# Kernel tuning notes

Measured on AMD Instinct MI355X. Metric: run time of the kernel, lower is better.

## Reference

```python
import jax, jax.numpy as jnp
import numpy as np

N = 50000      # nodes
R = 3          # relation types
E = 200000     # edges per relation
DIN, DHID, DOUT = 128, 128, 64


def _hetero_graphconv(x, src, dst, W, b):
    """Sum over relations of dgl GraphConv(norm='both') applied per relation.
    x:[N,d_in], src/dst:[R,E], W:[R,d_in,d_out], b:[R,d_out] -> [N,d_out]"""
    Rr, Ee = src.shape
    n = x.shape[0]
    off = (jnp.arange(Rr) * n)[:, None]            # per-relation segment offset
    src_f = (src + off).reshape(-1)                # [R*E]
    dst_f = (dst + off).reshape(-1)
    ones = jnp.ones((Rr * Ee,), x.dtype)
    out_deg = jax.ops.segment_sum(ones, src_f, num_segments=Rr * n).reshape(Rr, n)
    in_deg = jax.ops.segment_sum(ones, dst_f, num_segments=Rr * n).reshape(Rr, n)
    out_norm = jnp.maximum(out_deg, 1.0) ** -0.5   # dgl clamps deg to min 1
    in_norm = jnp.maximum(in_deg, 1.0) ** -0.5
    # gather src features, scaled by per-relation out-degree norm: [R,E,d_in]
    msgs = x[src] * jnp.take_along_axis(out_norm, src, axis=1)[..., None]
    agg = jax.ops.segment_sum(msgs.reshape(Rr * Ee, -1), dst_f,
                              num_segments=Rr * n).reshape(Rr, n, -1)
    agg = agg * in_norm[..., None]                 # [R,N,d_in]
    # per-relation linear then sum over relations (HeteroGraphConv 'sum')
    return jnp.einsum('rnd,rdo->no', agg, W) + b.sum(axis=0)


def setup_inputs() -> dict:
    key = jax.random.key(0)
    ks = jax.random.split(key, 7)
    x = jax.random.normal(ks[0], (N, DIN), jnp.float32)
    src = jax.random.randint(ks[1], (R, E), 0, N)
    dst = jax.random.randint(ks[2], (R, E), 0, N)
    W1 = jax.random.normal(ks[3], (R, DIN, DHID), jnp.float32) / np.sqrt(DIN).astype(np.float32)
    b1 = jax.random.normal(ks[4], (R, DHID), jnp.float32) * 0.01
    W2 = jax.random.normal(ks[5], (R, DHID, DOUT), jnp.float32) / np.sqrt(DHID).astype(np.float32)
    b2 = jax.random.normal(ks[6], (R, DOUT), jnp.float32) * 0.01
    return {"x": x, "W1": W1, "b1": b1, "W2": W2, "b2": b2, "src": src, "dst": dst}


def reference(x, W1, b1, W2, b2, src, dst):
    h = jax.nn.relu(_hetero_graphconv(x, src, dst, W1, b1))
    return _hetero_graphconv(h, src, dst, W2, b2)
```

## Files before the change

### kernel.cpp

```cpp
#include <hip/hip_runtime.h>

#define N_NODES 50000
#define N_REL   3
#define N_EDGE  200000
#define RN      (N_REL * N_NODES)
#define RE      (N_REL * N_EDGE)
#define GEMM1_BLKS 782
#define DEG_BLKS   2344
#define SCAN_BLOCKS 49
#define FUSE_CHUNKS 98

typedef short bf16x8 __attribute__((ext_vector_type(8)));
typedef float f32x4  __attribute__((ext_vector_type(4)));

__device__ __forceinline__ unsigned short f2bf(float f) {
    unsigned u = __float_as_uint(f);
    u = (u + 0x7fffu + ((u >> 16) & 1u)) >> 16;
    return (unsigned short)u;
}
__device__ __forceinline__ unsigned pack_bf2(float lo, float hi) {
    return (unsigned)f2bf(lo) | ((unsigned)f2bf(hi) << 16);
}

__device__ __forceinline__ void wtrans_one(
    const float* __restrict__ W, unsigned short* __restrict__ Wtf, int ncols, int i)
{
    int rel = i / (128 * ncols);
    int rem = i - rel * 128 * ncols;
    int k   = rem / ncols;
    int n   = rem - k * ncols;
    int f   = (rel * (ncols / 16) + (n >> 4)) * 4 + (k >> 5);
    int idx = f * 512 + ((k & 31) >> 3) * 128 + (n & 15) * 8 + (k & 7);
    Wtf[idx] = f2bf(W[i]);
}

__global__ __launch_bounds__(256) void wtrans2_kernel(
    const float* __restrict__ W1, unsigned short* __restrict__ Wt1,
    const float* __restrict__ W2, unsigned short* __restrict__ Wt2)
{
    int i = blockIdx.x * 256 + threadIdx.x;
    if (i < 3 * 128 * 128) {
        wtrans_one(W1, Wt1, 128, i);
    } else {
        int j = i - 3 * 128 * 128;
        if (j < 3 * 128 * 64) wtrans_one(W2, Wt2, 64, j);
    }
}

template <bool ABF16, int NCOLS>
__device__ __forceinline__ void gemm_body(
    const void* __restrict__ Av, const unsigned short* __restrict__ Wtf,
    unsigned short* __restrict__ Y, int nrows, int mt,
    unsigned* As, unsigned* Ws0, unsigned* Ws1)
{
    const int tid = threadIdx.x;
    const uint4* Wt4 = (const uint4*)Wtf;

    if constexpr (ABF16) {
        const uint4* Ab = (const uint4*)Av;
        #pragma unroll
        for (int p = 0; p < 4; ++p) {
            int q   = p * 256 + tid;
            int row = q >> 4, w4 = q & 15;
            int gr  = mt + row;
            uint4 v = make_uint4(0u, 0u, 0u, 0u);
            if (gr < nrows) v = Ab[(size_t)gr * 16 + w4];
            As[row * 68 + w4 * 4 + 0] = v.x;
            As[row * 68 + w4 * 4 + 1] = v.y;
            As[row * 68 + w4 * 4 + 2] = v.z;
            As[row * 68 + w4 * 4 + 3] = v.w;
        }
    } else {
        const float* A = (const float*)Av;
        #pragma unroll
        for (int p = 0; p < 16; ++p) {
            int q   = tid + p * 256;
            int row = q >> 6, wc = q & 63;
            int gr  = mt + row;
            float2 v = make_float2(0.f, 0.f);
            if (gr < nrows) v = *reinterpret_cast<const float2*>(&A[(size_t)gr * 128 + wc * 2]);
            As[row * 68 + wc] = pack_bf2(v.x, v.y);
        }
    }

    #pragma unroll
    for (int p = 0; p < 4; ++p) {
        uint4 v = Wt4[tid + p * 256];
        *reinterpret_cast<uint4*>(&Ws0[(tid + p * 256) * 4]) = v;
    }
    __syncthreads();

    const int w  = tid >> 6;
    const int l  = tid & 63;
    const int g  = l >> 4;
    const int lr = l & 15;
    const int ar = w * 16 + lr;

    bf16x8 a[4];
    #pragma unroll
    for (int kb = 0; kb < 4; ++kb)
        a[kb] = *reinterpret_cast<const bf16x8*>(&As[ar * 68 + kb * 16 + g * 4]);

    constexpr int TPR  = NCOLS / 16;
    constexpr int NGRP = 3 * NCOLS / 64;
    const int boff = (g * 16 + lr) * 4;

    unsigned* wc_buf = Ws0;
    unsigned* wn_buf = Ws1;
    #pragma unroll 1
    for (int grp = 0; grp < NGRP; ++grp) {
        uint4 st[4];
        if (grp + 1 < NGRP) {
            #pragma unroll
            for (int p = 0; p < 4; ++p)
                st[p] = Wt4[(grp + 1) * 1024 + tid + p * 256];
        }

        f32x4 acc[4];
        #pragma unroll
        for (int ct4 = 0; ct4 < 4; ++ct4) {
            acc[ct4] = (f32x4){0.f, 0.f, 0.f, 0.f};
            #pragma unroll
            for (int kb = 0; kb < 4; ++kb) {
                bf16x8 b = *reinterpret_cast<const bf16x8*>(
                    &wc_buf[(ct4 * 4 + kb) * 256 + boff]);
                acc[ct4] = __builtin_amdgcn_mfma_f32_16x16x32_bf16(a[kb], b, acc[ct4], 0, 0, 0);
            }
        }

        int gct0 = grp * 4;
        int rel  = gct0 / TPR;
        int cb   = (gct0 % TPR) * 16;
        #pragma unroll
        for (int i = 0; i < 4; ++i) {
            int grow = mt + w * 16 + g * 4 + i;
            if (grow < nrows) {
                size_t rowbase = ((size_t)rel * N_NODES + grow) * NCOLS + cb;
                #pragma unroll
                for (int ct4 = 0; ct4 < 4; ++ct4)
                    Y[rowbase + ct4 * 16 + lr] = f2bf(acc[ct4][i]);
            }
        }

        if (grp + 1 < NGRP) {
            #pragma unroll
            for (int p = 0; p < 4; ++p)
                *reinterpret_cast<uint4*>(&wn_buf[(tid + p * 256) * 4]) = st[p];
        }
        __syncthreads();
        unsigned* t = wc_buf; wc_buf = wn_buf; wn_buf = t;
    }
}

template <bool ABF16, int NCOLS>
__global__ __launch_bounds__(256) void gemm_mfma(
    const void* __restrict__ Av, const unsigned short* __restrict__ Wtf,
    unsigned short* __restrict__ Y, int nrows)
{
    __shared__ unsigned As[64 * 68];
    __shared__ unsigned Ws[2][4096];
    gemm_body<ABF16, NCOLS>(Av, Wtf, Y, nrows, blockIdx.x * 64, As, Ws[0], Ws[1]);
}

__device__ __forceinline__ void gemm1_body_light(
    const float* __restrict__ A, const unsigned short* __restrict__ Wtf,
    unsigned short* __restrict__ Y, int mt, unsigned* Ws)
{
    const int tid = threadIdx.x;
    const uint4* Wt4 = (const uint4*)Wtf;
    const int w  = tid >> 6;
    const int l  = tid & 63;
    const int g  = l >> 4;
    const int lr = l & 15;
    const int arow = mt + w * 16 + lr;
    const bool rowok = arow < N_NODES;

    bf16x8 a[4];
    #pragma unroll
    for (int kb = 0; kb < 4; ++kb) {
        float4 v0 = make_float4(0.f, 0.f, 0.f, 0.f);
        float4 v1 = make_float4(0.f, 0.f, 0.f, 0.f);
        if (rowok) {
            const float* ap = &A[(size_t)arow * 128 + kb * 32 + g * 8];
            v0 = *reinterpret_cast<const float4*>(ap);
            v1 = *reinterpret_cast<const float4*>(ap + 4);
        }
        union { unsigned u[4]; bf16x8 v; } cv;
        cv.u[0] = pack_bf2(v0.x, v0.y);
        cv.u[1] = pack_bf2(v0.z, v0.w);
        cv.u[2] = pack_bf2(v1.x, v1.y);
        cv.u[3] = pack_bf2(v1.z, v1.w);
        a[kb] = cv.v;
    }

    const int boff = (g * 16 + lr) * 4;

    #pragma unroll 1
    for (int grp = 0; grp < 6; ++grp) {
        __syncthreads();
        #pragma unroll
        for (int p = 0; p < 4; ++p) {
            uint4 v = Wt4[grp * 1024 + tid + p * 256];
            *reinterpret_cast<uint4*>(&Ws[(tid + p * 256) * 4]) = v;
        }
        __syncthreads();

        f32x4 acc[4];
        #pragma unroll
        for (int ct4 = 0; ct4 < 4; ++ct4) {
            acc[ct4] = (f32x4){0.f, 0.f, 0.f, 0.f};
            #pragma unroll
            for (int kb = 0; kb < 4; ++kb) {
                bf16x8 b = *reinterpret_cast<const bf16x8*>(
                    &Ws[(ct4 * 4 + kb) * 256 + boff]);
                acc[ct4] = __builtin_amdgcn_mfma_f32_16x16x32_bf16(a[kb], b, acc[ct4], 0, 0, 0);
            }
        }

        int rel = grp >> 1;
        int cb  = (grp & 1) * 64;
        #pragma unroll
        for (int i = 0; i < 4; ++i) {
            int grow = mt + w * 16 + g * 4 + i;
            if (grow < N_NODES) {
                size_t rowbase = ((size_t)rel * N_NODES + grow) * 128 + cb;
                #pragma unroll
                for (int ct4 = 0; ct4 < 4; ++ct4)
                    Y[rowbase + ct4 * 16 + lr] = f2bf(acc[ct4][i]);
            }
        }
    }
}

__global__ __launch_bounds__(256) void fused_gemm1_deg(
    const float* __restrict__ x, const unsigned short* __restrict__ Wt1,
    unsigned short* __restrict__ Y,
    const int* __restrict__ src, const int* __restrict__ dst,
    float* __restrict__ odeg, float* __restrict__ ideg,
    unsigned short* __restrict__ rank)
{
    __shared__ unsigned Ws[4096];

    const int c = blockIdx.x >> 5;
    const int o = blockIdx.x & 31;

    if (o < 8) {
        int gb = c * 8 + o;
        if (gb >= GEMM1_BLKS) return;
        gemm1_body_light(x, Wt1, Y, gb * 64, Ws);
    } else {
        int db = c * 24 + (o - 8);
        int i  = db * 256 + threadIdx.x;
        if (i < RE) {
            int r = i / N_EDGE;
            int s = src[i], t = dst[i];
            unsafeAtomicAdd(&odeg[r * N_NODES + s], 1.0f);
            float old = unsafeAtomicAdd(&ideg[r * N_NODES + t], 1.0f);
            rank[i] = (unsigned short)(int)old;
        }
    }
}

__global__ __launch_bounds__(256) void scan1_kernel(
    const float* __restrict__ ideg, int* __restrict__ off, int* __restrict__ bsums)
{
    __shared__ int tsum[256];
    int tid  = threadIdx.x;
    int base = blockIdx.x * 1024 + tid * 4;
    int c[4], s = 0;
    #pragma unroll
    for (int j = 0; j < 4; ++j) {
        int idx = base + j;
        c[j] = (idx < N_NODES)
             ? (int)(ideg[idx] + ideg[N_NODES + idx] + ideg[2 * N_NODES + idx]) : 0;
        s += c[j];
    }
    tsum[tid] = s;
    __syncthreads();
    #pragma unroll
    for (int d = 1; d < 256; d <<= 1) {
        int v   = tsum[tid];
        int add = (tid >= d) ? tsum[tid - d] : 0;
        __syncthreads();
        tsum[tid] = v + add;
        __syncthreads();
    }
    int run = tsum[tid] - s;
    #pragma unroll
    for (int j = 0; j < 4; ++j) {
        if (base + j < N_NODES) off[base + j] = run;
        run += c[j];
    }
    if (tid == 255) bsums[blockIdx.x] = tsum[255];
}

__global__ __launch_bounds__(256) void scan3_kernel(
    int* __restrict__ off, const int* __restrict__ bsums, int* __restrict__ roff,
    float* __restrict__ odeg, float* __restrict__ ideg)
{
    __shared__ int addsh;
    int tid = threadIdx.x;
    if (tid < 64) {
        int v = (tid < blockIdx.x) ? bsums[tid] : 0;
        #pragma unroll
        for (int d = 32; d > 0; d >>= 1) v += __shfl_down(v, d, 64);
        if (tid == 0) addsh = v;
    }
    __syncthreads();
    int add = addsh;

    int base = blockIdx.x * 1024 + tid * 4;
    #pragma unroll
    for (int j = 0; j < 4; ++j) {
        int t = base + j;
        if (t < N_NODES) {
            int v = off[t] + add;
            off[t] = v;
            float c0 = ideg[t];
            float c1 = ideg[N_NODES + t];
            float c2 = ideg[2 * N_NODES + t];
            roff[t]               = v;
            roff[N_NODES + t]     = v + (int)c0;
            roff[2 * N_NODES + t] = v + (int)(c0 + c1);
            ideg[t]               = rsqrtf(fmaxf(c0, 1.0f));
            ideg[N_NODES + t]     = rsqrtf(fmaxf(c1, 1.0f));
            ideg[2 * N_NODES + t] = rsqrtf(fmaxf(c2, 1.0f));
        }
    }
    if (blockIdx.x == 0 && tid == 0) off[N_NODES] = RE;

    int q0 = blockIdx.x * 256 + tid;
    for (int q = q0; q < RN; q += SCAN_BLOCKS * 256)
        odeg[q] = rsqrtf(fmaxf(odeg[q], 1.0f));
}

__global__ __launch_bounds__(256) void fill_kernel(
    const int* __restrict__ src, const int* __restrict__ dst,
    const float* __restrict__ onorm, const float* __restrict__ inorm,
    const int* __restrict__ roff, const unsigned short* __restrict__ rank,
    int2* __restrict__ csr)
{
    int i = blockIdx.x * 256 + threadIdx.x;
    if (i >= N_EDGE) return;
    int r   = blockIdx.y;
    int idx = r * N_EDGE + i;
    int s = src[idx], t = dst[idx];
    float wv = onorm[r * N_NODES + s] * inorm[r * N_NODES + t];
    int slot = roff[r * N_NODES + t] + (int)rank[idx];
    csr[slot] = make_int2(r * N_NODES + s, __float_as_int(wv));
}

__global__ __launch_bounds__(256) void agg128_kernel(
    const unsigned* __restrict__ Y, const int2* __restrict__ csr,
    const int* __restrict__ off, const float* __restrict__ b, unsigned* __restrict__ hbf)
{
    int wid  = (blockIdx.x * 256 + threadIdx.x) >> 6;
    int lane = threadIdx.x & 63;
    if (wid >= N_NODES) return;

    int e = off[wid], end = off[wid + 1];
    float a0 = 0.f, a1 = 0.f;

    for (; e + 8 <= end; e += 8) {
        int2 p[8]; unsigned y[8];
        #pragma unroll
        for (int j = 0; j < 8; ++j) p[j] = csr[e + j];
        #pragma unroll
        for (int j = 0; j < 8; ++j) y[j] = Y[(size_t)p[j].x * 64 + lane];
        #pragma unroll
        for (int j = 0; j < 8; ++j) {
            float wv = __int_as_float(p[j].y);
            a0 = fmaf(wv, __uint_as_float(y[j] << 16), a0);
            a1 = fmaf(wv, __uint_as_float(y[j] & 0xffff0000u), a1);
        }
    }
    if (e + 4 <= end) {
        int2 p[4]; unsigned y[4];
        #pragma unroll
        for (int j = 0; j < 4; ++j) p[j] = csr[e + j];
        #pragma unroll
        for (int j = 0; j < 4; ++j) y[j] = Y[(size_t)p[j].x * 64 + lane];
        #pragma unroll
        for (int j = 0; j < 4; ++j) {
            float wv = __int_as_float(p[j].y);
            a0 = fmaf(wv, __uint_as_float(y[j] << 16), a0);
            a1 = fmaf(wv, __uint_as_float(y[j] & 0xffff0000u), a1);
        }
        e += 4;
    }
    for (; e < end; ++e) {
        int2 p = csr[e];
        float wv = __int_as_float(p.y);
        unsigned y = Y[(size_t)p.x * 64 + lane];
        a0 = fmaf(wv, __uint_as_float(y << 16), a0);
        a1 = fmaf(wv, __uint_as_float(y & 0xffff0000u), a1);
    }

    int d = lane * 2;
    float o0 = a0 + b[d]     + b[128 + d]     + b[256 + d];
    float o1 = a1 + b[d + 1] + b[128 + d + 1] + b[256 + d + 1];
    hbf[(size_t)wid * 64 + lane] = pack_bf2(fmaxf(o0, 0.f), fmaxf(o1, 0.f));
}

__global__ __launch_bounds__(256) void agg64_kernel(
    const unsigned short* __restrict__ Y, const int2* __restrict__ csr,
    const int* __restrict__ off, const float* __restrict__ b, float* __restrict__ out)
{
    int wid  = (blockIdx.x * 256 + threadIdx.x) >> 6;
    int lane = threadIdx.x & 63;
    if (wid >= N_NODES) return;

    int e = off[wid], end = off[wid + 1];
    float a = 0.f;

    for (; e + 8 <= end; e += 8) {
        int2 p[8]; unsigned short y[8];
        #pragma unroll
        for (int j = 0; j < 8; ++j) p[j] = csr[e + j];
        #pragma unroll
        for (int j = 0; j < 8; ++j) y[j] = Y[(size_t)p[j].x * 64 + lane];
        #pragma unroll
        for (int j = 0; j < 8; ++j)
            a = fmaf(__int_as_float(p[j].y),
                     __uint_as_float(((unsigned)y[j]) << 16), a);
    }
    if (e + 4 <= end) {
        int2 p[4]; unsigned short y[4];
        #pragma unroll
        for (int j = 0; j < 4; ++j) p[j] = csr[e + j];
        #pragma unroll
        for (int j = 0; j < 4; ++j) y[j] = Y[(size_t)p[j].x * 64 + lane];
        #pragma unroll
        for (int j = 0; j < 4; ++j)
            a = fmaf(__int_as_float(p[j].y),
                     __uint_as_float(((unsigned)y[j]) << 16), a);
        e += 4;
    }
    for (; e < end; ++e) {
        int2 p = csr[e];
        a = fmaf(__int_as_float(p.y),
                 __uint_as_float(((unsigned)Y[(size_t)p.x * 64 + lane]) << 16), a);
    }

    float bs = b[lane] + b[64 + lane] + b[128 + lane];
    out[(size_t)wid * 64 + lane] = a + bs;
}

extern "C" void kernel_launch(void* const* d_in, const int* in_sizes, int n_in,
                              void* d_out, int out_size, void* d_ws, size_t ws_size,
                              hipStream_t stream)
{
    const float* x   = (const float*)d_in[0];
    const float* W1  = (const float*)d_in[1];
    const float* b1  = (const float*)d_in[2];
    const float* W2  = (const float*)d_in[3];
    const float* b2  = (const float*)d_in[4];
    const int*   src = (const int*)d_in[5];
    const int*   dst = (const int*)d_in[6];
    float*       out = (float*)d_out;

    char* w = (char*)d_ws;
    float* onorm  = (float*)w;                 w += (size_t)RN * 4;
    float* inorm  = (float*)w;                 w += (size_t)RN * 4;
    int*   off    = (int*)w;                   w += (size_t)(N_NODES + 1) * 4;
    int*   roff   = (int*)w;                   w += (size_t)RN * 4;
    int*   bsums  = (int*)w;                   w += 1024;
    unsigned short* rank = (unsigned short*)w; w += (size_t)RE * 2;
    w = (char*)(((uintptr_t)w + 255) & ~(uintptr_t)255);
    int2*  csr    = (int2*)w;                  w += (size_t)RE * 8;
    unsigned* hbf = (unsigned*)w;              w += (size_t)N_NODES * 64 * 4;
    unsigned short* Ybf = (unsigned short*)w;  w += (size_t)N_REL * N_NODES * 128 * 2;
    unsigned short* Wt1 = (unsigned short*)w;  w += (size_t)N_REL * 128 * 128 * 2;
    unsigned short* Wt2 = (unsigned short*)w;

    wtrans2_kernel<<<(3 * 128 * 128 + 3 * 128 * 64 + 255) / 256, 256, 0, stream>>>(
        W1, Wt1, W2, Wt2);

    hipMemsetAsync(onorm, 0, (size_t)2 * RN * 4, stream);
    fused_gemm1_deg<<<FUSE_CHUNKS * 32, 256, 0, stream>>>(
        x, Wt1, Ybf, src, dst, onorm, inorm, rank);

    scan1_kernel<<<SCAN_BLOCKS, 256, 0, stream>>>(inorm, off, bsums);
    scan3_kernel<<<SCAN_BLOCKS, 256, 0, stream>>>(off, bsums, roff, onorm, inorm);

    fill_kernel<<<dim3((N_EDGE + 255) / 256, N_REL), 256, 0, stream>>>(
        src, dst, onorm, inorm, roff, rank, csr);

    agg128_kernel<<<(N_NODES + 3) / 4, 256, 0, stream>>>((const unsigned*)Ybf, csr, off, b1, hbf);

    gemm_mfma<true, 64><<<GEMM1_BLKS, 256, 0, stream>>>(hbf, Wt2, Ybf, N_NODES);
    agg64_kernel<<<(N_NODES + 3) / 4, 256, 0, stream>>>(Ybf, csr, off, b2, out);
}
```

Before: 264.4 us.

## Pack CSR edges into 32 bits and fuse scans with grid barrier

```diff
diff --git a/kernel.cpp b/kernel.cpp
--- a/kernel.cpp
+++ b/kernel.cpp
@@ -9,6 +9,7 @@
 #define DEG_BLKS   2344
 #define SCAN_BLOCKS 49
 #define FUSE_CHUNKS 98
+#define PREP_BLKS  288
 
 typedef short bf16x8 __attribute__((ext_vector_type(8)));
 typedef float f32x4  __attribute__((ext_vector_type(4)));
@@ -34,11 +35,14 @@
     Wtf[idx] = f2bf(W[i]);
 }
 
-__global__ __launch_bounds__(256) void wtrans2_kernel(
+__global__ __launch_bounds__(256) void prep_kernel(
     const float* __restrict__ W1, unsigned short* __restrict__ Wt1,
-    const float* __restrict__ W2, unsigned short* __restrict__ Wt2)
+    const float* __restrict__ W2, unsigned short* __restrict__ Wt2,
+    float* __restrict__ zbuf, int* __restrict__ done)
 {
     int i = blockIdx.x * 256 + threadIdx.x;
+    if (i == 0) *done = 0;
+    for (int q = i; q < 2 * RN; q += PREP_BLKS * 256) zbuf[q] = 0.f;
     if (i < 3 * 128 * 128) {
         wtrans_one(W1, Wt1, 128, i);
     } else {
@@ -261,19 +265,28 @@
     }
 }
 
-__global__ __launch_bounds__(256) void scan1_kernel(
-    const float* __restrict__ ideg, int* __restrict__ off, int* __restrict__ bsums)
+__global__ __launch_bounds__(256) void scan_all_kernel(
+    float* __restrict__ odeg, float* __restrict__ ideg,
+    int* __restrict__ off, int* __restrict__ roff,
+    int* __restrict__ bsums, int* __restrict__ done)
 {
     __shared__ int tsum[256];
-    int tid  = threadIdx.x;
-    int base = blockIdx.x * 1024 + tid * 4;
-    int c[4], s = 0;
+    __shared__ int addsh;
+    const int tid  = threadIdx.x;
+    const int base = blockIdx.x * 1024 + tid * 4;
+
+    float c0[4], c1[4], c2[4];
+    int tot[4], s = 0;
     #pragma unroll
     for (int j = 0; j < 4; ++j) {
         int idx = base + j;
-        c[j] = (idx < N_NODES)
-             ? (int)(ideg[idx] + ideg[N_NODES + idx] + ideg[2 * N_NODES + idx]) : 0;
-        s += c[j];
+        if (idx < N_NODES) {
+            c0[j] = ideg[idx];
+            c1[j] = ideg[N_NODES + idx];
+            c2[j] = ideg[2 * N_NODES + idx];
+            tot[j] = (int)c0[j] + (int)c1[j] + (int)c2[j];
+        } else { c0[j] = c1[j] = c2[j] = 0.f; tot[j] = 0; }
+        s += tot[j];
     }
     tsum[tid] = s;
     __syncthreads();
@@ -286,20 +299,16 @@
         __syncthreads();
     }
     int run = tsum[tid] - s;
-    #pragma unroll
-    for (int j = 0; j < 4; ++j) {
-        if (base + j < N_NODES) off[base + j] = run;
-        run += c[j];
-    }
+
     if (tid == 255) bsums[blockIdx.x] = tsum[255];
-}
-
-__global__ __launch_bounds__(256) void scan3_kernel(
-    int* __restrict__ off, const int* __restrict__ bsums, int* __restrict__ roff,
-    float* __restrict__ odeg, float* __restrict__ ideg)
-{
-    __shared__ int addsh;
-    int tid = threadIdx.x;
+    __threadfence();
+    if (tid == 0) {
+        __hip_atomic_fetch_add(done, 1, __ATOMIC_RELEASE, __HIP_MEMORY_SCOPE_AGENT);
+        while (__hip_atomic_load(done, __ATOMIC_ACQUIRE, __HIP_MEMORY_SCOPE_AGENT) < SCAN_BLOCKS)
+            __builtin_amdgcn_s_sleep(2);
+    }
+    __syncthreads();
+
     if (tid < 64) {
         int v = (tid < blockIdx.x) ? bsums[tid] : 0;
         #pragma unroll
@@ -307,24 +316,20 @@
         if (tid == 0) addsh = v;
     }
     __syncthreads();
-    int add = addsh;
-
-    int base = blockIdx.x * 1024 + tid * 4;
+    int run2 = run + addsh;
+
     #pragma unroll
     for (int j = 0; j < 4; ++j) {
         int t = base + j;
         if (t < N_NODES) {
-            int v = off[t] + add;
-            off[t] = v;
-            float c0 = ideg[t];
-            float c1 = ideg[N_NODES + t];
-            float c2 = ideg[2 * N_NODES + t];
-            roff[t]               = v;
-            roff[N_NODES + t]     = v + (int)c0;
-            roff[2 * N_NODES + t] = v + (int)(c0 + c1);
-            ideg[t]               = rsqrtf(fmaxf(c0, 1.0f));
-            ideg[N_NODES + t]     = rsqrtf(fmaxf(c1, 1.0f));
-            ideg[2 * N_NODES + t] = rsqrtf(fmaxf(c2, 1.0f));
+            off[t]                = run2;
+            roff[t]               = run2;
+            roff[N_NODES + t]     = run2 + (int)c0[j];
+            roff[2 * N_NODES + t] = run2 + (int)c0[j] + (int)c1[j];
+            ideg[t]               = rsqrtf(fmaxf(c0[j], 1.0f));
+            ideg[N_NODES + t]     = rsqrtf(fmaxf(c1[j], 1.0f));
+            ideg[2 * N_NODES + t] = rsqrtf(fmaxf(c2[j], 1.0f));
+            run2 += tot[j];
         }
     }
     if (blockIdx.x == 0 && tid == 0) off[N_NODES] = RE;
@@ -338,7 +343,7 @@
     const int* __restrict__ src, const int* __restrict__ dst,
     const float* __restrict__ onorm, const float* __restrict__ inorm,
     const int* __restrict__ roff, const unsigned short* __restrict__ rank,
-    int2* __restrict__ csr)
+    unsigned* __restrict__ csr)
 {
     int i = blockIdx.x * 256 + threadIdx.x;
     if (i >= N_EDGE) return;
@@ -347,51 +352,61 @@
     int s = src[idx], t = dst[idx];
     float wv = onorm[r * N_NODES + s] * inorm[r * N_NODES + t];
     int slot = roff[r * N_NODES + t] + (int)rank[idx];
-    csr[slot] = make_int2(r * N_NODES + s, __float_as_int(wv));
+    csr[slot] = ((unsigned)s << 16) | (unsigned)f2bf(wv);
 }
 
 __global__ __launch_bounds__(256) void agg128_kernel(
-    const unsigned* __restrict__ Y, const int2* __restrict__ csr,
-    const int* __restrict__ off, const float* __restrict__ b, unsigned* __restrict__ hbf)
+    const unsigned* __restrict__ Y, const unsigned* __restrict__ csr,
+    const int* __restrict__ off, const int* __restrict__ roff,
+    const float* __restrict__ b, unsigned* __restrict__ hbf)
 {
     int wid  = (blockIdx.x * 256 + threadIdx.x) >> 6;
     int lane = threadIdx.x & 63;
     if (wid >= N_NODES) return;
 
-    int e = off[wid], end = off[wid + 1];
+    int e   = off[wid], end = off[wid + 1];
+    int r1  = roff[N_NODES + wid];
+    int r2  = roff[2 * N_NODES + wid];
     float a0 = 0.f, a1 = 0.f;
 
     for (; e + 8 <= end; e += 8) {
-        int2 p[8]; unsigned y[8];
+        unsigned p[8]; unsigned y[8];
         #pragma unroll
         for (int j = 0; j < 8; ++j) p[j] = csr[e + j];
         #pragma unroll
-        for (int j = 0; j < 8; ++j) y[j] = Y[(size_t)p[j].x * 64 + lane];
-        #pragma unroll
         for (int j = 0; j < 8; ++j) {
-            float wv = __int_as_float(p[j].y);
+            int rr = (e + j >= r1) + (e + j >= r2);
+            y[j] = Y[((size_t)rr * N_NODES + (p[j] >> 16)) * 64 + lane];
+        }
+        #pragma unroll
+        for (int j = 0; j < 8; ++j) {
+            float wv = __uint_as_float((p[j] & 0xffffu) << 16);
             a0 = fmaf(wv, __uint_as_float(y[j] << 16), a0);
             a1 = fmaf(wv, __uint_as_float(y[j] & 0xffff0000u), a1);
         }
     }
     if (e + 4 <= end) {
-        int2 p[4]; unsigned y[4];
+        unsigned p[4]; unsigned y[4];
         #pragma unroll
         for (int j = 0; j < 4; ++j) p[j] = csr[e + j];
         #pragma unroll
-        for (int j = 0; j < 4; ++j) y[j] = Y[(size_t)p[j].x * 64 + lane];
-        #pragma unroll
         for (int j = 0; j < 4; ++j) {
-            float wv = __int_as_float(p[j].y);
+            int rr = (e + j >= r1) + (e + j >= r2);
+            y[j] = Y[((size_t)rr * N_NODES + (p[j] >> 16)) * 64 + lane];
+        }
+        #pragma unroll
+        for (int j = 0; j < 4; ++j) {
+            float wv = __uint_as_float((p[j] & 0xffffu) << 16);
             a0 = fmaf(wv, __uint_as_float(y[j] << 16), a0);
             a1 = fmaf(wv, __uint_as_float(y[j] & 0xffff0000u), a1);
         }
         e += 4;
     }
     for (; e < end; ++e) {
-        int2 p = csr[e];
-        float wv = __int_as_float(p.y);
-        unsigned y = Y[(size_t)p.x * 64 + lane];
+        unsigned p = csr[e];
+        int rr = (e >= r1) + (e >= r2);
+        unsigned y = Y[((size_t)rr * N_NODES + (p >> 16)) * 64 + lane];
+        float wv = __uint_as_float((p & 0xffffu) << 16);
         a0 = fmaf(wv, __uint_as_float(y << 16), a0);
         a1 = fmaf(wv, __uint_as_float(y & 0xffff0000u), a1);
     }
@@ -403,43 +418,53 @@
 }
 
 __global__ __launch_bounds__(256) void agg64_kernel(
-    const unsigned short* __restrict__ Y, const int2* __restrict__ csr,
-    const int* __restrict__ off, const float* __restrict__ b, float* __restrict__ out)
+    const unsigned short* __restrict__ Y, const unsigned* __restrict__ csr,
+    const int* __restrict__ off, const int* __restrict__ roff,
+    const float* __restrict__ b, float* __restrict__ out)
 {
     int wid  = (blockIdx.x * 256 + threadIdx.x) >> 6;
     int lane = threadIdx.x & 63;
     if (wid >= N_NODES) return;
 
-    int e = off[wid], end = off[wid + 1];
+    int e   = off[wid], end = off[wid + 1];
+    int r1  = roff[N_NODES + wid];
+    int r2  = roff[2 * N_NODES + wid];
     float a = 0.f;
 
     for (; e + 8 <= end; e += 8) {
-        int2 p[8]; unsigned short y[8];
+        unsigned p[8]; unsigned short y[8];
         #pragma unroll
         for (int j = 0; j < 8; ++j) p[j] = csr[e + j];
         #pragma unroll
-        for (int j = 0; j < 8; ++j) y[j] = Y[(size_t)p[j].x * 64 + lane];
+        for (int j = 0; j < 8; ++j) {
+            int rr = (e + j >= r1) + (e + j >= r2);
+            y[j] = Y[((size_t)rr * N_NODES + (p[j] >> 16)) * 64 + lane];
+        }
         #pragma unroll
         for (int j = 0; j < 8; ++j)
-            a = fmaf(__int_as_float(p[j].y),
+            a = fmaf(__uint_as_float((p[j] & 0xffffu) << 16),
                      __uint_as_float(((unsigned)y[j]) << 16), a);
     }
     if (e + 4 <= end) {
-        int2 p[4]; unsigned short y[4];
+        unsigned p[4]; unsigned short y[4];
         #pragma unroll
         for (int j = 0; j < 4; ++j) p[j] = csr[e + j];
         #pragma unroll
-        for (int j = 0; j < 4; ++j) y[j] = Y[(size_t)p[j].x * 64 + lane];
+        for (int j = 0; j < 4; ++j) {
+            int rr = (e + j >= r1) + (e + j >= r2);
+            y[j] = Y[((size_t)rr * N_NODES + (p[j] >> 16)) * 64 + lane];
+        }
         #pragma unroll
         for (int j = 0; j < 4; ++j)
-            a = fmaf(__int_as_float(p[j].y),
+            a = fmaf(__uint_as_float((p[j] & 0xffffu) << 16),
                      __uint_as_float(((unsigned)y[j]) << 16), a);
         e += 4;
     }
     for (; e < end; ++e) {
-        int2 p = csr[e];
-        a = fmaf(__int_as_float(p.y),
-                 __uint_as_float(((unsigned)Y[(size_t)p.x * 64 + lane]) << 16), a);
+        unsigned p = csr[e];
+        int rr = (e >= r1) + (e >= r2);
+        a = fmaf(__uint_as_float((p & 0xffffu) << 16),
+                 __uint_as_float(((unsigned)Y[((size_t)rr * N_NODES + (p >> 16)) * 64 + lane]) << 16), a);
     }
 
     float bs = b[lane] + b[64 + lane] + b[128 + lane];
@@ -464,30 +489,29 @@
     float* inorm  = (float*)w;                 w += (size_t)RN * 4;
     int*   off    = (int*)w;                   w += (size_t)(N_NODES + 1) * 4;
     int*   roff   = (int*)w;                   w += (size_t)RN * 4;
-    int*   bsums  = (int*)w;                   w += 1024;
+    int*   bsums  = (int*)w;                   w += 512;
+    int*   done   = (int*)w;                   w += 512;
     unsigned short* rank = (unsigned short*)w; w += (size_t)RE * 2;
     w = (char*)(((uintptr_t)w + 255) & ~(uintptr_t)255);
-    int2*  csr    = (int2*)w;                  w += (size_t)RE * 8;
+    unsigned* csr = (unsigned*)w;              w += (size_t)RE * 4;
     unsigned* hbf = (unsigned*)w;              w += (size_t)N_NODES * 64 * 4;
     unsigned short* Ybf = (unsigned short*)w;  w += (size_t)N_REL * N_NODES * 128 * 2;
     unsigned short* Wt1 = (unsigned short*)w;  w += (size_t)N_REL * 128 * 128 * 2;
     unsigned short* Wt2 = (unsigned short*)w;
 
-    wtrans2_kernel<<<(3 * 128 * 128 + 3 * 128 * 64 + 255) / 256, 256, 0, stream>>>(
-        W1, Wt1, W2, Wt2);
-
-    hipMemsetAsync(onorm, 0, (size_t)2 * RN * 4, stream);
+    prep_kernel<<<PREP_BLKS, 256, 0, stream>>>(W1, Wt1, W2, Wt2, onorm, done);
+
     fused_gemm1_deg<<<FUSE_CHUNKS * 32, 256, 0, stream>>>(
         x, Wt1, Ybf, src, dst, onorm, inorm, rank);
 
-    scan1_kernel<<<SCAN_BLOCKS, 256, 0, stream>>>(inorm, off, bsums);
-    scan3_kernel<<<SCAN_BLOCKS, 256, 0, stream>>>(off, bsums, roff, onorm, inorm);
+    scan_all_kernel<<<SCAN_BLOCKS, 256, 0, stream>>>(onorm, inorm, off, roff, bsums, done);
 
     fill_kernel<<<dim3((N_EDGE + 255) / 256, N_REL), 256, 0, stream>>>(
         src, dst, onorm, inorm, roff, rank, csr);
 
-    agg128_kernel<<<(N_NODES + 3) / 4, 256, 0, stream>>>((const unsigned*)Ybf, csr, off, b1, hbf);
+    agg128_kernel<<<(N_NODES + 3) / 4, 256, 0, stream>>>(
+        (const unsigned*)Ybf, csr, off, roff, b1, hbf);
 
     gemm_mfma<true, 64><<<GEMM1_BLKS, 256, 0, stream>>>(hbf, Wt2, Ybf, N_NODES);
-    agg64_kernel<<<(N_NODES + 3) / 4, 256, 0, stream>>>(Ybf, csr, off, b2, out);
-}
+    agg64_kernel<<<(N_NODES + 3) / 4, 256, 0, stream>>>(Ybf, csr, off, roff, b2, out);
+}
```

Measured after the change: 261.2 us. No clear change (-1.2%).
